# Optimization experiments

Measured on AMD Instinct MI355X. Metric: run time of the kernel, lower is better.

The kernel has to match this reference:

```python
import jax, jax.numpy as jnp
import numpy as np

N_NODES = 50000
N_EDGES = 300000
D_IN = 256
D_HID = 256


def setup_inputs() -> dict:
    key = jax.random.key(0)
    ks = jax.random.split(key, 9)
    x = jax.random.normal(ks[0], (N_NODES, D_IN), dtype=jnp.float32)
    src = jax.random.randint(ks[1], (N_EDGES,), 0, N_NODES, dtype=jnp.int64)
    dst = jax.random.randint(ks[2], (N_EDGES,), 0, N_NODES, dtype=jnp.int64)
    # Kaiming-uniform-ish init like nn.Linear defaults
    def lin(k, fan_in, fan_out):
        bound = 1.0 / np.sqrt(fan_in)
        kw, kb = jax.random.split(k)
        W = jax.random.uniform(kw, (fan_out, fan_in), minval=-bound, maxval=bound, dtype=jnp.float32)
        b = jax.random.uniform(kb, (fan_out,), minval=-bound, maxval=bound, dtype=jnp.float32)
        return W, b
    W1, b1 = lin(ks[3], 2 * D_IN, D_HID)
    W2, b2 = lin(ks[4], D_HID, D_HID)
    W3, b3 = lin(ks[5], D_HID, 1)
    return {"x": x, "src": src, "dst": dst,
            "W1": W1, "b1": b1, "W2": W2, "b2": b2, "W3": W3, "b3": b3}


def reference(x, src, dst, W1, b1, W2, b2, W3, b3):
    # gather src/dst node features per edge and concat -> [E, 2*D_IN]
    h = jnp.concatenate([x[src], x[dst]], axis=1)
    h = jax.nn.relu(h @ W1.T + b1)          # [E, D_HID]
    h = jax.nn.relu(h @ W2.T + b2)          # dropout is identity in eval mode
    score = h @ W3.T + b3                   # [E, 1]
    return score
```

## Files before the change

kernel.cpp:

```cpp
#include <hip/hip_runtime.h>

typedef short bfx8 __attribute__((ext_vector_type(8)));
typedef float fx4 __attribute__((ext_vector_type(4)));

#define D 256
#define E_TILE 64

__device__ __forceinline__ float b2f(short s) {
  union { unsigned u; float f; } v; v.u = ((unsigned)(unsigned short)s) << 16; return v.f;
}
__device__ __forceinline__ short f2b(float f) {
  union { float f; unsigned u; } v; v.f = f;
  unsigned u = v.u;
  u += 0x7fffu + ((u >> 16) & 1u);
  return (short)(u >> 16);
}
__device__ __forceinline__ float relu(float f) { return f > 0.f ? f : 0.f; }

__global__ void k_prep(const float* __restrict__ W1, const float* __restrict__ W2,
                       unsigned short* __restrict__ B1, unsigned short* __restrict__ W2b) {
  int t = blockIdx.x * 256 + threadIdx.x;
  if (t < 512 * 256) {
    int n = t >> 8, k = t & 255;
    float v = (n < 256) ? W1[n * 512 + k] : W1[(n - 256) * 512 + 256 + k];
    B1[t] = (unsigned short)f2b(v);
  } else if (t < 512 * 256 + 256 * 256) {
    int i = t - 512 * 256;
    W2b[i] = (unsigned short)f2b(W2[i]);
  }
}

__launch_bounds__(256, 2)
__global__ void k_node(const float* __restrict__ x, const unsigned short* __restrict__ B1,
                       unsigned short* __restrict__ PQ, int n_nodes) {
  __shared__ __align__(16) short smA[64 * 40];
  __shared__ __align__(16) short smW[512 * 40];
  short* smT = smW;
  const int tid = threadIdx.x;
  const int wave = tid >> 6, lane = tid & 63;
  const int lr = lane & 15, lg = lane >> 4;
  const int m0 = blockIdx.x * 64;

  fx4 acc[4][8] = {};

#pragma unroll 1
  for (int ks = 0; ks < 8; ++ks) {
    const int k0 = ks * 32;
    {
      int r = tid >> 2, c = (tid & 3) * 8;
      int m = m0 + r;
      bfx8 o;
      if (m < n_nodes) {
        const float* p = x + (size_t)m * 256 + k0 + c;
        float4 v0 = *(const float4*)(p);
        float4 v1 = *(const float4*)(p + 4);
        o[0] = f2b(v0.x); o[1] = f2b(v0.y); o[2] = f2b(v0.z); o[3] = f2b(v0.w);
        o[4] = f2b(v1.x); o[5] = f2b(v1.y); o[6] = f2b(v1.z); o[7] = f2b(v1.w);
      } else {
        o = (bfx8){0,0,0,0,0,0,0,0};
      }
      *(bfx8*)&smA[r * 40 + c] = o;
    }
#pragma unroll
    for (int it = 0; it < 8; ++it) {
      int idx = it * 256 + tid;
      int n = idx >> 2, c = (idx & 3) * 8;
      bfx8 v = *(const bfx8*)(B1 + n * 256 + k0 + c);
      *(bfx8*)&smW[n * 40 + c] = v;
    }
    __syncthreads();
    bfx8 af[4];
#pragma unroll
    for (int mt = 0; mt < 4; ++mt)
      af[mt] = *(const bfx8*)&smA[(mt * 16 + lr) * 40 + lg * 8];
#pragma unroll
    for (int nt = 0; nt < 8; ++nt) {
      int n = wave * 128 + nt * 16 + lr;
      bfx8 bf = *(const bfx8*)&smW[n * 40 + lg * 8];
#pragma unroll
      for (int mt = 0; mt < 4; ++mt)
        acc[mt][nt] = __builtin_amdgcn_mfma_f32_16x16x32_bf16(af[mt], bf, acc[mt][nt], 0, 0, 0);
    }
    __syncthreads();
  }

#pragma unroll
  for (int h = 0; h < 2; ++h) {
#pragma unroll
    for (int mt2 = 0; mt2 < 2; ++mt2) {
      const int mt = 2 * h + mt2;
#pragma unroll
      for (int nt = 0; nt < 8; ++nt)
#pragma unroll
        for (int i = 0; i < 4; ++i) {
          int mrow = mt2 * 16 + lg * 4 + i;
          int n = wave * 128 + nt * 16 + lr;
          smT[mrow * 520 + n] = f2b(acc[mt][nt][i]);
        }
    }
    __syncthreads();
    int r = tid >> 3, cbase = (tid & 7) * 8;
    int m = m0 + h * 32 + r;
    if (m < n_nodes) {
#pragma unroll
      for (int j = 0; j < 8; ++j) {
        int c = cbase + j * 64;
        *(bfx8*)(PQ + (size_t)m * 512 + c) = *(const bfx8*)&smT[r * 520 + c];
      }
    }
    __syncthreads();
  }
}

__launch_bounds__(256, 2)
__global__ void k_edge(const unsigned short* __restrict__ PQ,
                       const int* __restrict__ src, const int* __restrict__ dst,
                       const float* __restrict__ b1, const unsigned short* __restrict__ W2b,
                       const float* __restrict__ b2, const float* __restrict__ W3,
                       const float* __restrict__ b3, float* __restrict__ out,
                       int E, int ntiles) {
  __shared__ __align__(16) short smH[64 * 264];
  __shared__ float smS[4][64];
  __shared__ float smB1[256];
  const int tid = threadIdx.x;
  const int wave = tid >> 6, lane = tid & 63;
  const int lr = lane & 15, lg = lane >> 4;

  if (tid < 256) smB1[tid] = b1[tid];

  bfx8 bw[4][8];
  float b2v[4], w3v[4];
#pragma unroll
  for (int nt = 0; nt < 4; ++nt) {
    int n = wave * 64 + nt * 16 + lr;
    b2v[nt] = b2[n];
    w3v[nt] = W3[n];
#pragma unroll
    for (int ks = 0; ks < 8; ++ks)
      bw[nt][ks] = *(const bfx8*)(W2b + n * 256 + ks * 32 + lg * 8);
  }
  const float b3v = b3[0];
  __syncthreads();

  for (int tile = blockIdx.x; tile < ntiles; tile += gridDim.x) {
    const int base = tile * E_TILE;
    {
      int r = tid >> 2;
      int e = base + r;
      if (e < E) {
        int s = src[e], d = dst[e];
        const unsigned short* ps = PQ + (size_t)s * 512;
        const unsigned short* pd = PQ + (size_t)d * 512 + 256;
#pragma unroll
        for (int it = 0; it < 8; ++it) {
          int c = (tid & 3) * 8 + it * 32;
          bfx8 pv = *(const bfx8*)(ps + c);
          bfx8 qv = *(const bfx8*)(pd + c);
          bfx8 o;
#pragma unroll
          for (int j = 0; j < 8; ++j)
            o[j] = f2b(relu(b2f(pv[j]) + b2f(qv[j]) + smB1[c + j]));
          *(bfx8*)&smH[r * 264 + c] = o;
        }
      } else {
        bfx8 z = (bfx8){0,0,0,0,0,0,0,0};
#pragma unroll
        for (int it = 0; it < 8; ++it) {
          int c = (tid & 3) * 8 + it * 32;
          *(bfx8*)&smH[r * 264 + c] = z;
        }
      }
    }
    __syncthreads();

    fx4 acc[4][4] = {};
#pragma unroll
    for (int ks = 0; ks < 8; ++ks) {
      bfx8 af[4];
#pragma unroll
      for (int mt = 0; mt < 4; ++mt)
        af[mt] = *(const bfx8*)&smH[(mt * 16 + lr) * 264 + ks * 32 + lg * 8];
#pragma unroll
      for (int nt = 0; nt < 4; ++nt)
#pragma unroll
        for (int mt = 0; mt < 4; ++mt)
          acc[mt][nt] = __builtin_amdgcn_mfma_f32_16x16x32_bf16(af[mt], bw[nt][ks], acc[mt][nt], 0, 0, 0);
    }

#pragma unroll
    for (int mt = 0; mt < 4; ++mt)
#pragma unroll
      for (int i = 0; i < 4; ++i) {
        float p = 0.f;
#pragma unroll
        for (int nt = 0; nt < 4; ++nt)
          p += relu(acc[mt][nt][i] + b2v[nt]) * w3v[nt];
        p += __shfl_xor(p, 1);
        p += __shfl_xor(p, 2);
        p += __shfl_xor(p, 4);
        p += __shfl_xor(p, 8);
        if (lr == 0) smS[wave][mt * 16 + lg * 4 + i] = p;
      }
    __syncthreads();
    if (tid < 64) {
      int e = base + tid;
      if (e < E) out[e] = smS[0][tid] + smS[1][tid] + smS[2][tid] + smS[3][tid] + b3v;
    }
    __syncthreads();
  }
}

__global__ void k_fallback(const float* __restrict__ x, const int* __restrict__ src,
                           const int* __restrict__ dst, const float* __restrict__ W1,
                           const float* __restrict__ b1, const float* __restrict__ W2,
                           const float* __restrict__ b2, const float* __restrict__ W3,
                           const float* __restrict__ b3, float* __restrict__ out, int E) {
  __shared__ float smF[4][512];
  __shared__ float smG[4][256];
  int wave = threadIdx.x >> 6, lane = threadIdx.x & 63;
  int e = blockIdx.x * 4 + wave;
  bool valid = e < E;
  int ec = valid ? e : 0;
  int s = src[ec], d = dst[ec];
  for (int j = 0; j < 8; ++j) {
    int k = lane * 8 + j;
    smF[wave][k] = (k < 256) ? x[(size_t)s * 256 + k] : x[(size_t)d * 256 + k - 256];
  }
  __syncthreads();
  for (int t = 0; t < 4; ++t) {
    int n = lane + t * 64;
    float a = b1[n];
    for (int k = 0; k < 512; ++k) a += smF[wave][k] * W1[n * 512 + k];
    smG[wave][n] = relu(a);
  }
  __syncthreads();
  float p = 0.f;
  for (int t = 0; t < 4; ++t) {
    int n = lane + t * 64;
    float a = b2[n];
    for (int k = 0; k < 256; ++k) a += smG[wave][k] * W2[n * 256 + k];
    p += relu(a) * W3[n];
  }
  for (int m = 1; m < 64; m <<= 1) p += __shfl_xor(p, m);
  if (lane == 0 && valid) out[e] = p + b3[0];
}

extern "C" void kernel_launch(void* const* d_in, const int* in_sizes, int n_in,
                              void* d_out, int out_size, void* d_ws, size_t ws_size,
                              hipStream_t stream) {
  const float* x  = (const float*)d_in[0];
  const int*   src = (const int*)d_in[1];
  const int*   dst = (const int*)d_in[2];
  const float* W1 = (const float*)d_in[3];
  const float* b1 = (const float*)d_in[4];
  const float* W2 = (const float*)d_in[5];
  const float* b2 = (const float*)d_in[6];
  const float* W3 = (const float*)d_in[7];
  const float* b3 = (const float*)d_in[8];
  float* out = (float*)d_out;

  const int E = in_sizes[1];
  const int n_nodes = in_sizes[0] / 256;

  const size_t offB1 = 0;
  const size_t offW2 = (size_t)512 * 256 * 2;
  const size_t offPQ = offW2 + (size_t)256 * 256 * 2;
  const size_t need = offPQ + (size_t)n_nodes * 512 * 2;

  if (ws_size >= need) {
    unsigned short* B1  = (unsigned short*)((char*)d_ws + offB1);
    unsigned short* W2b = (unsigned short*)((char*)d_ws + offW2);
    unsigned short* PQ  = (unsigned short*)((char*)d_ws + offPQ);
    k_prep<<<768, 256, 0, stream>>>(W1, W2, B1, W2b);
    k_node<<<(n_nodes + 63) / 64, 256, 0, stream>>>(x, B1, PQ, n_nodes);
    const int ntiles = (E + E_TILE - 1) / E_TILE;
    k_edge<<<512, 256, 0, stream>>>(PQ, src, dst, b1, W2b, b2, W3, b3, out, E, ntiles);
  } else {
    k_fallback<<<(E + 3) / 4, 256, 0, stream>>>(x, src, dst, W1, b1, W2, b2, W3, b3, out, E);
  }
}
```

Measured before the change: 215.3 us.

## Restructure node GEMM to stage full x tile once, read B1 from global, fold b1

The node-projection kernel now converts the whole 64x256 x tile into shared memory once, then computes the two 256-column halves of the output in turn. B1 weight fragments are read directly from global/L2 instead of being staged through shared memory every k-step, which removes the per-k-step barriers and shrinks the accumulator set. The b1 bias is folded into the Q half of the node output so the edge kernel no longer loads or adds it per element. The risk is extra global latency on B1 loads inside the MFMA loop in exchange for less LDS traffic and synchronization.

```diff
diff --git a/kernel.cpp b/kernel.cpp
--- a/kernel.cpp
+++ b/kernel.cpp
@@ -3,7 +3,6 @@
 typedef short bfx8 __attribute__((ext_vector_type(8)));
 typedef float fx4 __attribute__((ext_vector_type(4)));
 
-#define D 256
 #define E_TILE 64
 
 __device__ __forceinline__ float b2f(short s) {
@@ -32,101 +31,105 @@
 
 __launch_bounds__(256, 2)
 __global__ void k_node(const float* __restrict__ x, const unsigned short* __restrict__ B1,
+                       const float* __restrict__ b1,
                        unsigned short* __restrict__ PQ, int n_nodes) {
-  __shared__ __align__(16) short smA[64 * 40];
-  __shared__ __align__(16) short smW[512 * 40];
-  short* smT = smW;
+  __shared__ __align__(16) short smA[64 * 264];
+  __shared__ __align__(16) short smT[32 * 264];
   const int tid = threadIdx.x;
   const int wave = tid >> 6, lane = tid & 63;
   const int lr = lane & 15, lg = lane >> 4;
   const int m0 = blockIdx.x * 64;
 
-  fx4 acc[4][8] = {};
-
-#pragma unroll 1
-  for (int ks = 0; ks < 8; ++ks) {
-    const int k0 = ks * 32;
-    {
-      int r = tid >> 2, c = (tid & 3) * 8;
-      int m = m0 + r;
+  {
+    int r = tid >> 2;
+    int m = m0 + r;
+    bool ok = m < n_nodes;
+#pragma unroll
+    for (int j = 0; j < 8; ++j) {
+      int c = (tid & 3) * 8 + j * 32;
       bfx8 o;
-      if (m < n_nodes) {
-        const float* p = x + (size_t)m * 256 + k0 + c;
+      if (ok) {
+        const float* p = x + (size_t)m * 256 + c;
         float4 v0 = *(const float4*)(p);
         float4 v1 = *(const float4*)(p + 4);
         o[0] = f2b(v0.x); o[1] = f2b(v0.y); o[2] = f2b(v0.z); o[3] = f2b(v0.w);
         o[4] = f2b(v1.x); o[5] = f2b(v1.y); o[6] = f2b(v1.z); o[7] = f2b(v1.w);
       } else {
-        o = (bfx8){0,0,0,0,0,0,0,0};
-      }
-      *(bfx8*)&smA[r * 40 + c] = o;
-    }
-#pragma unroll
-    for (int it = 0; it < 8; ++it) {
-      int idx = it * 256 + tid;
-      int n = idx >> 2, c = (idx & 3) * 8;
-      bfx8 v = *(const bfx8*)(B1 + n * 256 + k0 + c);
-      *(bfx8*)&smW[n * 40 + c] = v;
-    }
-    __syncthreads();
-    bfx8 af[4];
-#pragma unroll
-    for (int mt = 0; mt < 4; ++mt)
-      af[mt] = *(const bfx8*)&smA[(mt * 16 + lr) * 40 + lg * 8];
-#pragma unroll
-    for (int nt = 0; nt < 8; ++nt) {
-      int n = wave * 128 + nt * 16 + lr;
-      bfx8 bf = *(const bfx8*)&smW[n * 40 + lg * 8];
+        o = (bfx8){0, 0, 0, 0, 0, 0, 0, 0};
+      }
+      *(bfx8*)&smA[r * 264 + c] = o;
+    }
+  }
+  __syncthreads();
+
+#pragma unroll
+  for (int half = 0; half < 2; ++half) {
+    const int n0 = half * 256 + wave * 64;
+
+    fx4 acc[4][4] = {};
+#pragma unroll
+    for (int ks = 0; ks < 8; ++ks) {
+      bfx8 af[4];
 #pragma unroll
       for (int mt = 0; mt < 4; ++mt)
-        acc[mt][nt] = __builtin_amdgcn_mfma_f32_16x16x32_bf16(af[mt], bf, acc[mt][nt], 0, 0, 0);
-    }
-    __syncthreads();
-  }
-
-#pragma unroll
-  for (int h = 0; h < 2; ++h) {
-#pragma unroll
-    for (int mt2 = 0; mt2 < 2; ++mt2) {
-      const int mt = 2 * h + mt2;
-#pragma unroll
-      for (int nt = 0; nt < 8; ++nt)
-#pragma unroll
-        for (int i = 0; i < 4; ++i) {
-          int mrow = mt2 * 16 + lg * 4 + i;
-          int n = wave * 128 + nt * 16 + lr;
-          smT[mrow * 520 + n] = f2b(acc[mt][nt][i]);
+        af[mt] = *(const bfx8*)&smA[(mt * 16 + lr) * 264 + ks * 32 + lg * 8];
+#pragma unroll
+      for (int nt = 0; nt < 4; ++nt) {
+        bfx8 bf = *(const bfx8*)(B1 + (size_t)(n0 + nt * 16 + lr) * 256 + ks * 32 + lg * 8);
+#pragma unroll
+        for (int mt = 0; mt < 4; ++mt)
+          acc[mt][nt] = __builtin_amdgcn_mfma_f32_16x16x32_bf16(af[mt], bf, acc[mt][nt], 0, 0, 0);
+      }
+    }
+
+    float bias[4];
+#pragma unroll
+    for (int nt = 0; nt < 4; ++nt) {
+      int n = n0 + nt * 16 + lr;
+      bias[nt] = half ? b1[n - 256] : 0.f;
+    }
+
+#pragma unroll
+    for (int h = 0; h < 2; ++h) {
+      __syncthreads();
+#pragma unroll
+      for (int mt2 = 0; mt2 < 2; ++mt2) {
+        const int mt = 2 * h + mt2;
+#pragma unroll
+        for (int nt = 0; nt < 4; ++nt)
+#pragma unroll
+          for (int i = 0; i < 4; ++i) {
+            int mr = mt2 * 16 + lg * 4 + i;
+            int nc = wave * 64 + nt * 16 + lr;
+            smT[mr * 264 + nc] = f2b(acc[mt][nt][i] + bias[nt]);
+          }
+      }
+      __syncthreads();
+      int r = tid >> 3, cbase = (tid & 7) * 8;
+      int m = m0 + h * 32 + r;
+      if (m < n_nodes) {
+#pragma unroll
+        for (int j = 0; j < 4; ++j) {
+          int c = cbase + j * 64;
+          *(bfx8*)(PQ + (size_t)m * 512 + half * 256 + c) = *(const bfx8*)&smT[r * 264 + c];
         }
-    }
-    __syncthreads();
-    int r = tid >> 3, cbase = (tid & 7) * 8;
-    int m = m0 + h * 32 + r;
-    if (m < n_nodes) {
-#pragma unroll
-      for (int j = 0; j < 8; ++j) {
-        int c = cbase + j * 64;
-        *(bfx8*)(PQ + (size_t)m * 512 + c) = *(const bfx8*)&smT[r * 520 + c];
-      }
-    }
-    __syncthreads();
+      }
+    }
   }
 }
 
 __launch_bounds__(256, 2)
 __global__ void k_edge(const unsigned short* __restrict__ PQ,
                        const int* __restrict__ src, const int* __restrict__ dst,
-                       const float* __restrict__ b1, const unsigned short* __restrict__ W2b,
+                       const unsigned short* __restrict__ W2b,
                        const float* __restrict__ b2, const float* __restrict__ W3,
                        const float* __restrict__ b3, float* __restrict__ out,
                        int E, int ntiles) {
   __shared__ __align__(16) short smH[64 * 264];
   __shared__ float smS[4][64];
-  __shared__ float smB1[256];
   const int tid = threadIdx.x;
   const int wave = tid >> 6, lane = tid & 63;
   const int lr = lane & 15, lg = lane >> 4;
-
-  if (tid < 256) smB1[tid] = b1[tid];
 
   bfx8 bw[4][8];
   float b2v[4], w3v[4];
@@ -140,7 +143,6 @@
       bw[nt][ks] = *(const bfx8*)(W2b + n * 256 + ks * 32 + lg * 8);
   }
   const float b3v = b3[0];
-  __syncthreads();
 
   for (int tile = blockIdx.x; tile < ntiles; tile += gridDim.x) {
     const int base = tile * E_TILE;
@@ -159,11 +161,11 @@
           bfx8 o;
 #pragma unroll
           for (int j = 0; j < 8; ++j)
-            o[j] = f2b(relu(b2f(pv[j]) + b2f(qv[j]) + smB1[c + j]));
+            o[j] = f2b(relu(b2f(pv[j]) + b2f(qv[j])));
           *(bfx8*)&smH[r * 264 + c] = o;
         }
       } else {
-        bfx8 z = (bfx8){0,0,0,0,0,0,0,0};
+        bfx8 z = (bfx8){0, 0, 0, 0, 0, 0, 0, 0};
 #pragma unroll
         for (int it = 0; it < 8; ++it) {
           int c = (tid & 3) * 8 + it * 32;
@@ -272,9 +274,9 @@
     unsigned short* W2b = (unsigned short*)((char*)d_ws + offW2);
     unsigned short* PQ  = (unsigned short*)((char*)d_ws + offPQ);
     k_prep<<<768, 256, 0, stream>>>(W1, W2, B1, W2b);
-    k_node<<<(n_nodes + 63) / 64, 256, 0, stream>>>(x, B1, PQ, n_nodes);
+    k_node<<<(n_nodes + 63) / 64, 256, 0, stream>>>(x, B1, b1, PQ, n_nodes);
     const int ntiles = (E + E_TILE - 1) / E_TILE;
-    k_edge<<<512, 256, 0, stream>>>(PQ, src, dst, b1, W2b, b2, W3, b3, out, E, ntiles);
+    k_edge<<<512, 256, 0, stream>>>(PQ, src, dst, W2b, b2, W3, b3, out, E, ntiles);
   } else {
     k_fallback<<<(E + 3) / 4, 256, 0, stream>>>(x, src, dst, W1, b1, W2, b2, W3, b3, out, E);
   }
```

Result: slower. 219.7 us (+2.0%).
